# Kernel tuning notes

Hardware: AMD Instinct MI355X
Metric: run time of the kernel (lower is better)

Reference implementation:

```python
import jax, jax.numpy as jnp
import numpy as np

B, C, T = 8, 512, 1024
H = 8
D = C // H          # head_dim = 64
K = 64              # max_rel_dist
REL = 2 * K + 1     # 129


def setup_inputs() -> dict:
    key = jax.random.key(0)
    ks = jax.random.split(key, 12)
    s = 0.02
    return {
        "x": jax.random.normal(ks[0], (B, C, T), jnp.float32),
        "x_mask": jnp.ones((B, 1, T), jnp.float32),
        "W_q": jax.random.normal(ks[1], (C, C), jnp.float32) * s,
        "b_q": jnp.zeros((C,), jnp.float32),
        "W_k": jax.random.normal(ks[2], (C, C), jnp.float32) * s,
        "b_k": jnp.zeros((C,), jnp.float32),
        "W_v": jax.random.normal(ks[3], (C, C), jnp.float32) * s,
        "b_v": jnp.zeros((C,), jnp.float32),
        "W_o": jax.random.normal(ks[4], (C, C), jnp.float32) * s,
        "b_o": jnp.zeros((C,), jnp.float32),
        "emb_rel_k": jax.random.normal(ks[5], (REL, D), jnp.float32) * 0.01,
        "emb_rel_v": jax.random.normal(ks[6], (REL, D), jnp.float32) * 0.01,
    }


def _conv1x1(x, W, b):
    # Conv1d with kernel_size=1: (B,C,T) x (Cout,Cin) -> (B,Cout,T)
    return jnp.einsum("oc,bct->bot", W, x) + b[None, :, None]


def _shape_heads(x):
    # (B,C,T) -> (B,H,T,D)
    b = x.shape[0]
    return x.reshape(b, H, D, T).transpose(0, 1, 3, 2)


def reference(x, x_mask, W_q, b_q, W_k, b_k, W_v, b_v, W_o, b_o, emb_rel_k, emb_rel_v):
    q = _shape_heads(_conv1x1(x, W_q, b_q))  # (B,H,T,D)
    k = _shape_heads(_conv1x1(x, W_k, b_k))
    v = _shape_heads(_conv1x1(x, W_v, b_v))

    # relative position indices: clamp(j - i, -K, K) + K  -> (T,T)
    pos = jnp.arange(T)
    rel_idx = jnp.clip(pos[None, :] - pos[:, None], -K, K) + K

    # scores: scaled QK^T plus unscaled relative-key term (faithful to source)
    attn = jnp.einsum("bhid,bhjd->bhij", q, k) / (D ** 0.5)
    rel_k_tt = emb_rel_k[rel_idx]            # (T,T,D)
    attn = attn + jnp.einsum("bhid,ijd->bhij", q, rel_k_tt)

    # key mask: positions with x_mask <= 0 get -1e9
    key_mask = (x_mask <= 0).reshape(x.shape[0], 1, 1, T)
    attn = jnp.where(key_mask, -1e9, attn)
    attn = jax.nn.softmax(attn, axis=-1)     # dropout p=0.0 -> identity

    y = jnp.einsum("bhij,bhjd->bhid", attn, v)
    rel_v_tt = emb_rel_v[rel_idx]            # (T,T,D)
    y = y + jnp.einsum("bhij,ijd->bhid", attn, rel_v_tt)

    # (B,H,T,D) -> (B,H,D,T) -> (B,C,T)
    y = y.transpose(0, 1, 3, 2).reshape(x.shape[0], C, T)
    y = _conv1x1(y, W_o, b_o)
    return y * x_mask
```

## Files before the change

kernel.cpp:

```cpp
#include <hip/hip_runtime.h>

#define B_   8
#define C_   512
#define T_   1024
#define H_   8
#define D_   64
#define K_   64
#define REL_ 129

typedef unsigned short u16;
typedef __attribute__((ext_vector_type(8))) short short8;
typedef __attribute__((ext_vector_type(4))) float f32x4;

__device__ __forceinline__ float b2f(u16 u) {
    return __uint_as_float(((unsigned)u) << 16);
}
__device__ __forceinline__ u16 f2b(float f) {
    unsigned x = __float_as_uint(f);
    x += 0x7fffu + ((x >> 16) & 1u);
    return (u16)(x >> 16);
}

__global__ __launch_bounds__(256) void cast_all_kernel(
    const float* __restrict__ x,
    const float* __restrict__ Wq, const float* __restrict__ Wk,
    const float* __restrict__ Wv, const float* __restrict__ Wo,
    const float* __restrict__ erk, const float* __restrict__ erv,
    u16* __restrict__ xt, u16* __restrict__ Wh,
    u16* __restrict__ ervt, u16* __restrict__ erkb)
{
    __shared__ u16 tile[64][72];
    const int blk = blockIdx.x;
    const int tid = threadIdx.x;
    if (blk < 1024) {
        const int t0 = (blk & 15) * 64, c0 = ((blk >> 4) & 7) * 64, b = blk >> 7;
        const int f = tid & 15, r0 = tid >> 4;
#pragma unroll
        for (int p = 0; p < 4; ++p) {
            const int c = r0 + p * 16;
            const float4 v = *(const float4*)(x + ((size_t)b * C_ + c0 + c) * T_ + t0 + f * 4);
            tile[c][f * 4 + 0] = f2b(v.x);
            tile[c][f * 4 + 1] = f2b(v.y);
            tile[c][f * 4 + 2] = f2b(v.z);
            tile[c][f * 4 + 3] = f2b(v.w);
        }
        __syncthreads();
#pragma unroll
        for (int p = 0; p < 4; ++p) {
            const int t = r0 + p * 16;
            ushort4 u;
            u.x = tile[f * 4 + 0][t];
            u.y = tile[f * 4 + 1][t];
            u.z = tile[f * 4 + 2][t];
            u.w = tile[f * 4 + 3][t];
            *(ushort4*)(xt + ((size_t)b * T_ + t0 + t) * C_ + c0 + f * 4) = u;
        }
    } else if (blk < 2048) {
        const int gid = (blk - 1024) * 256 + tid;
        const int s = gid >> 16;
        const int off = (gid & 65535) * 4;
        const float* W = (s == 0) ? Wq : (s == 1) ? Wk : (s == 2) ? Wv : Wo;
        const float4 v = *(const float4*)(W + off);
        ushort4 u;
        u.x = f2b(v.x); u.y = f2b(v.y); u.z = f2b(v.z); u.w = f2b(v.w);
        *(ushort4*)(Wh + ((size_t)s << 18) + off) = u;
    } else {
        const int idx = (blk - 2048) * 256 + tid;
        if (idx < 64 * 160) {
            const int d = idx / 160, rel = idx % 160;
            ervt[idx] = (rel < REL_) ? f2b(erv[rel * D_ + d]) : (u16)0;
        } else {
            const int j = idx - 64 * 160;
            if (j < REL_ * D_) erkb[j] = f2b(erk[j]);
        }
    }
}

__global__ __launch_bounds__(256) void proj_mfma(
    const u16* __restrict__ xt, const u16* __restrict__ Wh,
    const float* __restrict__ bq, const float* __restrict__ bk, const float* __restrict__ bv,
    u16* __restrict__ qh, u16* __restrict__ kh, u16* __restrict__ vt)
{
    __shared__ u16 Wt[64][72];

    const int t0 = blockIdx.x * 64;
    const int h  = blockIdx.y;
    const int sel = blockIdx.z >> 3;
    const int b   = blockIdx.z & 7;
    const int tid = threadIdx.x, wave = tid >> 6, lane = tid & 63;
    const int quad = lane >> 4, l16 = lane & 15;

    const u16* Wbase = Wh + ((size_t)sel << 18) + ((size_t)(h * 64) << 9);
    const u16* A = xt + (((size_t)b * T_ + t0 + wave * 16 + l16) << 9);

    const int so = tid >> 2;
    const int sc = (tid & 3) * 16;
    const u16* wsrc = Wbase + ((size_t)so << 9) + sc;

    f32x4 acc[4] = {{0.f,0.f,0.f,0.f},{0.f,0.f,0.f,0.f},{0.f,0.f,0.f,0.f},{0.f,0.f,0.f,0.f}};

    uint4 wv0 = *(const uint4*)(wsrc);
    uint4 wv1 = *(const uint4*)(wsrc + 8);
#pragma unroll 1
    for (int i = 0; i < 8; ++i) {
        const int c0 = i * 64;
        __syncthreads();
        *(uint4*)&Wt[so][sc] = wv0;
        *(uint4*)&Wt[so][sc + 8] = wv1;
        __syncthreads();
        if (i < 7) {
            wv0 = *(const uint4*)(wsrc + c0 + 64);
            wv1 = *(const uint4*)(wsrc + c0 + 72);
        }
#pragma unroll
        for (int kk = 0; kk < 64; kk += 32) {
            const short8 af = *(const short8*)(A + c0 + kk + quad * 8);
#pragma unroll
            for (int nt = 0; nt < 4; ++nt) {
                const short8 bf = *(const short8*)(&Wt[nt * 16 + l16][kk + quad * 8]);
                acc[nt] = __builtin_amdgcn_mfma_f32_16x16x32_bf16(af, bf, acc[nt], 0, 0, 0);
            }
        }
    }

    const float* bias = (sel == 0) ? bq : (sel == 1) ? bk : bv;
    const int bh = b * 8 + h;
#pragma unroll
    for (int nt = 0; nt < 4; ++nt) {
        const int d = nt * 16 + l16;
        const float bo = bias[h * 64 + d];
#pragma unroll
        for (int rix = 0; rix < 4; ++rix) {
            const int t = t0 + wave * 16 + quad * 4 + rix;
            const u16 val = f2b(acc[nt][rix] + bo);
            if (sel == 2) {
                vt[(((size_t)bh * 64 + d) << 10) + t] = val;
            } else {
                u16* dst = sel ? kh : qh;
                dst[(((size_t)bh * T_ + t) << 6) + d] = val;
            }
        }
    }
}

__global__ __launch_bounds__(256, 2) void attn_kernel(
    const u16* __restrict__ qh, const u16* __restrict__ kh, const u16* __restrict__ vt,
    const u16* __restrict__ erkb, const u16* __restrict__ ervt,
    const float* __restrict__ xmask, u16* __restrict__ yf)
{
    __shared__ u16   Sb[32][1032];
    __shared__ u16   sw[32][168];
    __shared__ float red[4][32][2];
    __shared__ float invrow[32];

    const int gid = blockIdx.x;
    const int x8 = gid & 7, r5 = gid >> 3;
    const int bh = x8 + 8 * (r5 >> 5);
    const int i0 = (r5 & 31) * 32;
    const int b = bh >> 3, h = bh & 7;
    const int tid = threadIdx.x, wave = tid >> 6, lane = tid & 63;
    const int quad = lane >> 4, l16 = lane & 15;

    short8 qa[2][2];
#pragma unroll
    for (int g = 0; g < 2; ++g) {
        const u16* qrow = qh + (((size_t)bh * T_ + i0 + g * 16 + l16) << 6);
        qa[g][0] = *(const short8*)(qrow + quad * 8);
        qa[g][1] = *(const short8*)(qrow + 32 + quad * 8);
    }

    for (int tile = wave; tile < 9; tile += 4) {
        const int rel = tile * 16 + l16;
        const int rl = rel > 128 ? 128 : rel;
        const u16* ep = erkb + rl * 64 + quad * 8;
        const short8 b0 = *(const short8*)(ep);
        const short8 b1 = *(const short8*)(ep + 32);
#pragma unroll
        for (int g = 0; g < 2; ++g) {
            f32x4 m = {0.f, 0.f, 0.f, 0.f};
            m = __builtin_amdgcn_mfma_f32_16x16x32_bf16(qa[g][0], b0, m, 0, 0, 0);
            m = __builtin_amdgcn_mfma_f32_16x16x32_bf16(qa[g][1], b1, m, 0, 0, 0);
            if (rel < 129) {
#pragma unroll
                for (int rix = 0; rix < 4; ++rix)
                    sw[g * 16 + quad * 4 + rix][rel] = f2b(m[rix]);
            }
        }
    }
    __syncthreads();

    float slo_c[2][4], shi_c[2][4];
#pragma unroll
    for (int g = 0; g < 2; ++g)
#pragma unroll
        for (int rix = 0; rix < 4; ++rix) {
            const int row = g * 16 + quad * 4 + rix;
            slo_c[g][rix] = b2f(sw[row][0]);
            shi_c[g][rix] = b2f(sw[row][2 * K_]);
        }

    float psum[2][4] = {{0.f,0.f,0.f,0.f},{0.f,0.f,0.f,0.f}};
    float phi [2][4] = {{0.f,0.f,0.f,0.f},{0.f,0.f,0.f,0.f}};
    f32x4 og[4][2];
#pragma unroll
    for (int s = 0; s < 4; ++s)
#pragma unroll
        for (int g = 0; g < 2; ++g) og[s][g] = (f32x4){0.f, 0.f, 0.f, 0.f};

    {
        const u16* kb = kh + ((size_t)bh << 16);
        const u16* vbase = vt + ((size_t)bh << 16);
#pragma unroll 1
        for (int c = 0; c < 8; ++c) {
#pragma unroll
            for (int half = 0; half < 2; ++half) {
                const int ct = c * 2 + half;
                const int j0 = wave * 256 + ct * 16;
                const u16* krow = kb + ((size_t)(j0 + l16) << 6);
                const short8 kb0 = *(const short8*)(krow + quad * 8);
                const short8 kb1 = *(const short8*)(krow + 32 + quad * 8);
                const int j = j0 + l16;
                const float xmv = xmask[b * T_ + j];
#pragma unroll
                for (int g = 0; g < 2; ++g) {
                    f32x4 acc = {0.f, 0.f, 0.f, 0.f};
                    acc = __builtin_amdgcn_mfma_f32_16x16x32_bf16(qa[g][0], kb0, acc, 0, 0, 0);
                    acc = __builtin_amdgcn_mfma_f32_16x16x32_bf16(qa[g][1], kb1, acc, 0, 0, 0);
                    const int dd = j0 - (i0 + g * 16);
                    if (dd <= -79) {
#pragma unroll
                        for (int rix = 0; rix < 4; ++rix) {
                            const int row = g * 16 + quad * 4 + rix;
                            float val = acc[rix] * 0.125f + slo_c[g][rix];
                            val = (xmv > 0.f) ? val : -1e9f;
                            const u16 pb = f2b(__expf(fminf(val, 30.f)));
                            const float er = b2f(pb);
                            Sb[row][j] = pb;
                            psum[g][rix] += er;
                        }
                    } else if (dd >= 79) {
#pragma unroll
                        for (int rix = 0; rix < 4; ++rix) {
                            const int row = g * 16 + quad * 4 + rix;
                            float val = acc[rix] * 0.125f + shi_c[g][rix];
                            val = (xmv > 0.f) ? val : -1e9f;
                            const u16 pb = f2b(__expf(fminf(val, 30.f)));
                            const float er = b2f(pb);
                            Sb[row][j] = pb;
                            psum[g][rix] += er;
                            phi[g][rix]  += er;
                        }
                    } else {
#pragma unroll
                        for (int rix = 0; rix < 4; ++rix) {
                            const int row = g * 16 + quad * 4 + rix;
                            const int i = i0 + row;
                            int rel = j - i;
                            rel = (rel < -K_) ? -K_ : (rel > K_) ? K_ : rel;
                            float val = acc[rix] * 0.125f + b2f(sw[row][rel + K_]);
                            val = (xmv > 0.f) ? val : -1e9f;
                            const u16 pb = f2b(__expf(fminf(val, 30.f)));
                            const float er = b2f(pb);
                            Sb[row][j] = pb;
                            psum[g][rix] += er;
                            phi[g][rix]  += (j >= i + K_) ? er : 0.f;
                        }
                    }
                }
            }
            const int kc = wave * 256 + c * 32;
            const short8 pb0 = *(const short8*)(&Sb[l16][kc + quad * 8]);
            const short8 pb1 = *(const short8*)(&Sb[16 + l16][kc + quad * 8]);
#pragma unroll
            for (int s = 0; s < 4; ++s) {
                const short8 af = *(const short8*)(vbase + ((size_t)(s * 16 + l16) << 10) + kc + quad * 8);
                og[s][0] = __builtin_amdgcn_mfma_f32_16x16x32_bf16(af, pb0, og[s][0], 0, 0, 0);
                og[s][1] = __builtin_amdgcn_mfma_f32_16x16x32_bf16(af, pb1, og[s][1], 0, 0, 0);
            }
        }
#pragma unroll
        for (int m = 1; m < 16; m <<= 1)
#pragma unroll
            for (int g = 0; g < 2; ++g)
#pragma unroll
                for (int rix = 0; rix < 4; ++rix) {
                    psum[g][rix] += __shfl_xor(psum[g][rix], m);
                    phi[g][rix]  += __shfl_xor(phi[g][rix], m);
                }
        if (l16 == 0)
#pragma unroll
            for (int g = 0; g < 2; ++g)
#pragma unroll
                for (int rix = 0; rix < 4; ++rix) {
                    const int row = g * 16 + quad * 4 + rix;
                    red[wave][row][0] = psum[g][rix];
                    red[wave][row][1] = phi[g][rix];
                }
    }
    __syncthreads();

    {
        const int rr = tid >> 3;
        const int c0 = tid & 7;
        const float sumrow = red[0][rr][0] + red[1][rr][0] + red[2][rr][0] + red[3][rr][0];
        const float phirow = red[0][rr][1] + red[1][rr][1] + red[2][rr][1] + red[3][rr][1];
        float intsum = 0.f;
        for (int rel = c0; rel < 168; rel += 8) {
            if (rel == 0 || rel == 2 * K_) continue;
            u16 v = 0;
            if (rel < 2 * K_) {
                const int j = i0 + rr + rel - K_;
                if (j >= 0 && j < T_) v = Sb[rr][j];
                intsum += b2f(v);
            }
            sw[rr][rel] = v;
        }
        intsum += __shfl_xor(intsum, 1);
        intsum += __shfl_xor(intsum, 2);
        intsum += __shfl_xor(intsum, 4);
        if (c0 == 0) {
            sw[rr][2 * K_] = f2b(phirow);
            sw[rr][0]      = f2b(sumrow - intsum - phirow);
            invrow[rr]     = 1.0f / sumrow;
        }
    }
    __syncthreads();

    float* fog = (float*)&Sb[0][0];
#pragma unroll
    for (int s = 0; s < 4; ++s)
#pragma unroll
        for (int g = 0; g < 2; ++g)
            *(f32x4*)&fog[wave * 2048 + ((s * 2 + g) * 64 + lane) * 4] = og[s][g];
    __syncthreads();

    {
        const int dh = wave * 16 + l16;
        const u16* ep = ervt + dh * 160;
        f32x4 accg[2];
#pragma unroll
        for (int g = 0; g < 2; ++g) {
            const int base = ((wave * 2 + g) * 64 + lane) * 4;
            f32x4 a0 = *(const f32x4*)&fog[base];
            f32x4 a1 = *(const f32x4*)&fog[2048 + base];
            f32x4 a2 = *(const f32x4*)&fog[4096 + base];
            f32x4 a3 = *(const f32x4*)&fog[6144 + base];
#pragma unroll
            for (int rix = 0; rix < 4; ++rix)
                accg[g][rix] = (a0[rix] + a1[rix]) + (a2[rix] + a3[rix]);
        }
#pragma unroll
        for (int kt = 0; kt < 5; ++kt) {
            const short8 af = *(const short8*)(ep + kt * 32 + quad * 8);
            const short8 p0 = *(const short8*)(&sw[l16][kt * 32 + quad * 8]);
            const short8 p1 = *(const short8*)(&sw[16 + l16][kt * 32 + quad * 8]);
            accg[0] = __builtin_amdgcn_mfma_f32_16x16x32_bf16(af, p0, accg[0], 0, 0, 0);
            accg[1] = __builtin_amdgcn_mfma_f32_16x16x32_bf16(af, p1, accg[1], 0, 0, 0);
        }
        const int dbase = (h << 6) + wave * 16 + quad * 4;
#pragma unroll
        for (int g = 0; g < 2; ++g) {
            const float iv = invrow[g * 16 + l16];
            ushort4 u;
            u.x = f2b(accg[g][0] * iv); u.y = f2b(accg[g][1] * iv);
            u.z = f2b(accg[g][2] * iv); u.w = f2b(accg[g][3] * iv);
            *(ushort4*)(yf + (((size_t)b * T_ + i0 + g * 16 + l16) << 9) + dbase) = u;
        }
    }
}

__global__ __launch_bounds__(256) void outproj_mfma(
    const u16* __restrict__ yf, const u16* __restrict__ Woh, const float* __restrict__ bo,
    const float* __restrict__ xmask, float* __restrict__ out)
{
    __shared__ u16 Yt[64][72];

    const int o0 = blockIdx.x * 64;
    const int b  = blockIdx.y >> 4;
    const int t0 = (blockIdx.y & 15) * 64;
    const int tid = threadIdx.x, wave = tid >> 6, lane = tid & 63;
    const int quad = lane >> 4, l16 = lane & 15;

    const u16* A = Woh + ((size_t)(o0 + wave * 16 + l16) << 9);

    const int so = tid >> 2;
    const int sc = (tid & 3) * 16;
    const u16* ysrc = yf + (((size_t)b * T_ + t0 + so) << 9) + sc;

    f32x4 acc[4] = {{0.f,0.f,0.f,0.f},{0.f,0.f,0.f,0.f},{0.f,0.f,0.f,0.f},{0.f,0.f,0.f,0.f}};

    uint4 wv0 = *(const uint4*)(ysrc);
    uint4 wv1 = *(const uint4*)(ysrc + 8);
#pragma unroll 1
    for (int i = 0; i < 8; ++i) {
        const int c0 = i * 64;
        __syncthreads();
        *(uint4*)&Yt[so][sc] = wv0;
        *(uint4*)&Yt[so][sc + 8] = wv1;
        __syncthreads();
        if (i < 7) {
            wv0 = *(const uint4*)(ysrc + c0 + 64);
            wv1 = *(const uint4*)(ysrc + c0 + 72);
        }
#pragma unroll
        for (int kk = 0; kk < 64; kk += 32) {
            const short8 af = *(const short8*)(A + c0 + kk + quad * 8);
#pragma unroll
            for (int nt = 0; nt < 4; ++nt) {
                const short8 bf = *(const short8*)(&Yt[nt * 16 + l16][kk + quad * 8]);
                acc[nt] = __builtin_amdgcn_mfma_f32_16x16x32_bf16(af, bf, acc[nt], 0, 0, 0);
            }
        }
    }

#pragma unroll
    for (int nt = 0; nt < 4; ++nt) {
        const int t = t0 + nt * 16 + l16;
        const float xmv = xmask[b * T_ + t];
#pragma unroll
        for (int rix = 0; rix < 4; ++rix) {
            const int o = o0 + wave * 16 + quad * 4 + rix;
            out[((size_t)b * C_ + o) * T_ + t] = (acc[nt][rix] + bo[o]) * xmv;
        }
    }
}

extern "C" void kernel_launch(void* const* d_in, const int* in_sizes, int n_in,
                              void* d_out, int out_size, void* d_ws, size_t ws_size,
                              hipStream_t stream) {
    const float* x     = (const float*)d_in[0];
    const float* xmask = (const float*)d_in[1];
    const float* Wq    = (const float*)d_in[2];
    const float* bq    = (const float*)d_in[3];
    const float* Wk    = (const float*)d_in[4];
    const float* bk    = (const float*)d_in[5];
    const float* Wv    = (const float*)d_in[6];
    const float* bv    = (const float*)d_in[7];
    const float* Wo    = (const float*)d_in[8];
    const float* bo    = (const float*)d_in[9];
    const float* erk   = (const float*)d_in[10];
    const float* erv   = (const float*)d_in[11];

    const size_t need = 44077184;
    if (ws_size < need) return;
    u16* xt   = (u16*)d_ws;
    u16* Wh   = (u16*)((char*)d_ws + 8388608);
    u16* qh   = (u16*)((char*)d_ws + 10485760);
    u16* kh   = (u16*)((char*)d_ws + 18874368);
    u16* vt   = (u16*)((char*)d_ws + 27262976);
    u16* yf   = (u16*)((char*)d_ws + 35651584);
    u16* ervt = (u16*)((char*)d_ws + 44040192);
    u16* erkb = (u16*)((char*)d_ws + 44060672);
    float* out = (float*)d_out;

    cast_all_kernel<<<dim3(2121), 256, 0, stream>>>(
        x, Wq, Wk, Wv, Wo, erk, erv, xt, Wh, ervt, erkb);
    proj_mfma<<<dim3(T_ / 64, H_, 3 * B_), 256, 0, stream>>>(
        xt, Wh, bq, bk, bv, qh, kh, vt);
    attn_kernel<<<dim3(2048), 256, 0, stream>>>(
        qh, kh, vt, erkb, ervt, xmask, yf);
    outproj_mfma<<<dim3(C_ / 64, B_ * (T_ / 64)), 256, 0, stream>>>(
        yf, Wh + ((size_t)3 << 18), bo, xmask, out);
}
```

Before: 237.5 us.

## Shrink attention LDS to a diagonal band plus per-wave scratch for higher occupancy

New measurement: 281.5 us. 18.5% more time.

```diff
diff --git a/kernel.cpp b/kernel.cpp
--- a/kernel.cpp
+++ b/kernel.cpp
@@ -143,15 +143,18 @@
     }
 }
 
-__global__ __launch_bounds__(256, 2) void attn_kernel(
+__global__ __launch_bounds__(256, 4) void attn_kernel(
     const u16* __restrict__ qh, const u16* __restrict__ kh, const u16* __restrict__ vt,
     const u16* __restrict__ erkb, const u16* __restrict__ ervt,
     const float* __restrict__ xmask, u16* __restrict__ yf)
 {
-    __shared__ u16   Sb[32][1032];
+    __shared__ __align__(16) char pool[10752 + 10240];
     __shared__ u16   sw[32][168];
     __shared__ float red[4][32][2];
     __shared__ float invrow[32];
+
+    u16 (*Sband)[168]   = (u16 (*)[168])pool;
+    u16 (*scr)[32][40]  = (u16 (*)[32][40])(pool + 10752);
 
     const int gid = blockIdx.x;
     const int x8 = gid & 7, r5 = gid >> 3;
@@ -183,7 +186,7 @@
             if (rel < 129) {
 #pragma unroll
                 for (int rix = 0; rix < 4; ++rix)
-                    sw[g * 16 + quad * 4 + rix][rel] = f2b(m[rix]);
+                    sw[g * 16 + quad * 4 + rix][rel] = f2b(m[rix] * 1.4426950408889634f);
             }
         }
     }
@@ -210,12 +213,14 @@
     {
         const u16* kb = kh + ((size_t)bh << 16);
         const u16* vbase = vt + ((size_t)bh << 16);
+        const int bandlo = i0 - 64, bandhi = i0 + 96;
 #pragma unroll 1
         for (int c = 0; c < 8; ++c) {
+            const int jc = wave * 256 + c * 32;
+            const bool inband = (jc >= bandlo) && (jc < bandhi);
 #pragma unroll
             for (int half = 0; half < 2; ++half) {
-                const int ct = c * 2 + half;
-                const int j0 = wave * 256 + ct * 16;
+                const int j0 = jc + half * 16;
                 const u16* krow = kb + ((size_t)(j0 + l16) << 6);
                 const short8 kb0 = *(const short8*)(krow + quad * 8);
                 const short8 kb1 = *(const short8*)(krow + 32 + quad * 8);
@@ -227,53 +232,37 @@
                     acc = __builtin_amdgcn_mfma_f32_16x16x32_bf16(qa[g][0], kb0, acc, 0, 0, 0);
                     acc = __builtin_amdgcn_mfma_f32_16x16x32_bf16(qa[g][1], kb1, acc, 0, 0, 0);
                     const int dd = j0 - (i0 + g * 16);
-                    if (dd <= -79) {
-#pragma unroll
-                        for (int rix = 0; rix < 4; ++rix) {
-                            const int row = g * 16 + quad * 4 + rix;
-                            float val = acc[rix] * 0.125f + slo_c[g][rix];
-                            val = (xmv > 0.f) ? val : -1e9f;
-                            const u16 pb = f2b(__expf(fminf(val, 30.f)));
-                            const float er = b2f(pb);
-                            Sb[row][j] = pb;
-                            psum[g][rix] += er;
-                        }
-                    } else if (dd >= 79) {
-#pragma unroll
-                        for (int rix = 0; rix < 4; ++rix) {
-                            const int row = g * 16 + quad * 4 + rix;
-                            float val = acc[rix] * 0.125f + shi_c[g][rix];
-                            val = (xmv > 0.f) ? val : -1e9f;
-                            const u16 pb = f2b(__expf(fminf(val, 30.f)));
-                            const float er = b2f(pb);
-                            Sb[row][j] = pb;
-                            psum[g][rix] += er;
-                            phi[g][rix]  += er;
-                        }
-                    } else {
-#pragma unroll
-                        for (int rix = 0; rix < 4; ++rix) {
-                            const int row = g * 16 + quad * 4 + rix;
-                            const int i = i0 + row;
+#pragma unroll
+                    for (int rix = 0; rix < 4; ++rix) {
+                        const int row = g * 16 + quad * 4 + rix;
+                        const int i = i0 + row;
+                        float sr;
+                        if (dd <= -79) sr = slo_c[g][rix];
+                        else if (dd >= 79) sr = shi_c[g][rix];
+                        else {
                             int rel = j - i;
                             rel = (rel < -K_) ? -K_ : (rel > K_) ? K_ : rel;
-                            float val = acc[rix] * 0.125f + b2f(sw[row][rel + K_]);
-                            val = (xmv > 0.f) ? val : -1e9f;
-                            const u16 pb = f2b(__expf(fminf(val, 30.f)));
-                            const float er = b2f(pb);
-                            Sb[row][j] = pb;
-                            psum[g][rix] += er;
-                            phi[g][rix]  += (j >= i + K_) ? er : 0.f;
+                            sr = b2f(sw[row][rel + K_]);
                         }
+                        float val = acc[rix] * 0.18033688011112042f + sr;
+                        val = (xmv > 0.f) ? val : -1e9f;
+                        const u16 pb = f2b(exp2f(val));
+                        const float er = b2f(pb);
+                        if (inband) Sband[row][j - i0 + 64] = pb;
+                        else        scr[wave][row][half * 16 + l16] = pb;
+                        psum[g][rix] += er;
+                        if (dd >= 79)      phi[g][rix] += er;
+                        else if (dd > -79) phi[g][rix] += (j >= i + K_) ? er : 0.f;
                     }
                 }
             }
-            const int kc = wave * 256 + c * 32;
-            const short8 pb0 = *(const short8*)(&Sb[l16][kc + quad * 8]);
-            const short8 pb1 = *(const short8*)(&Sb[16 + l16][kc + quad * 8]);
+            const u16* pr0 = inband ? &Sband[l16][jc - i0 + 64]      : &scr[wave][l16][0];
+            const u16* pr1 = inband ? &Sband[16 + l16][jc - i0 + 64] : &scr[wave][16 + l16][0];
+            const short8 pb0 = *(const short8*)(pr0 + quad * 8);
+            const short8 pb1 = *(const short8*)(pr1 + quad * 8);
 #pragma unroll
             for (int s = 0; s < 4; ++s) {
-                const short8 af = *(const short8*)(vbase + ((size_t)(s * 16 + l16) << 10) + kc + quad * 8);
+                const short8 af = *(const short8*)(vbase + ((size_t)(s * 16 + l16) << 10) + jc + quad * 8);
                 og[s][0] = __builtin_amdgcn_mfma_f32_16x16x32_bf16(af, pb0, og[s][0], 0, 0, 0);
                 og[s][1] = __builtin_amdgcn_mfma_f32_16x16x32_bf16(af, pb1, og[s][1], 0, 0, 0);
             }
@@ -310,7 +299,7 @@
             u16 v = 0;
             if (rel < 2 * K_) {
                 const int j = i0 + rr + rel - K_;
-                if (j >= 0 && j < T_) v = Sb[rr][j];
+                if (j >= 0 && j < T_) v = Sband[rr][rr + rel];
                 intsum += b2f(v);
             }
             sw[rr][rel] = v;
@@ -326,29 +315,36 @@
     }
     __syncthreads();
 
-    float* fog = (float*)&Sb[0][0];
-#pragma unroll
-    for (int s = 0; s < 4; ++s)
-#pragma unroll
-        for (int g = 0; g < 2; ++g)
-            *(f32x4*)&fog[wave * 2048 + ((s * 2 + g) * 64 + lane) * 4] = og[s][g];
-    __syncthreads();
+    float* ogbuf = (float*)pool;
+    f32x4 accg[2];
+#pragma unroll 1
+    for (int r = 0; r < 2; ++r) {
+        if (r) __syncthreads();
+#pragma unroll
+        for (int sl = 0; sl < 2; ++sl)
+#pragma unroll
+            for (int g = 0; g < 2; ++g)
+                *(f32x4*)&ogbuf[((wave * 4 + sl * 2 + g) * 64 + lane) * 4] = og[2 * r + sl][g];
+        __syncthreads();
+        if ((wave >> 1) == r) {
+            const int sl = wave & 1;
+#pragma unroll
+            for (int g = 0; g < 2; ++g) {
+                const int base = ((sl * 2 + g) * 64 + lane) * 4;
+                const f32x4 a0 = *(const f32x4*)&ogbuf[base];
+                const f32x4 a1 = *(const f32x4*)&ogbuf[1024 + base];
+                const f32x4 a2 = *(const f32x4*)&ogbuf[2048 + base];
+                const f32x4 a3 = *(const f32x4*)&ogbuf[3072 + base];
+#pragma unroll
+                for (int rix = 0; rix < 4; ++rix)
+                    accg[g][rix] = (a0[rix] + a1[rix]) + (a2[rix] + a3[rix]);
+            }
+        }
+    }
 
     {
         const int dh = wave * 16 + l16;
         const u16* ep = ervt + dh * 160;
-        f32x4 accg[2];
-#pragma unroll
-        for (int g = 0; g < 2; ++g) {
-            const int base = ((wave * 2 + g) * 64 + lane) * 4;
-            f32x4 a0 = *(const f32x4*)&fog[base];
-            f32x4 a1 = *(const f32x4*)&fog[2048 + base];
-            f32x4 a2 = *(const f32x4*)&fog[4096 + base];
-            f32x4 a3 = *(const f32x4*)&fog[6144 + base];
-#pragma unroll
-            for (int rix = 0; rix < 4; ++rix)
-                accg[g][rix] = (a0[rix] + a1[rix]) + (a2[rix] + a3[rix]);
-        }
 #pragma unroll
         for (int kt = 0; kt < 5; ++kt) {
             const short8 af = *(const short8*)(ep + kt * 32 + quad * 8);
```
